# Kernel optimization log

Measured on AMD Instinct MI355X. Metric: run time of the kernel, lower is better.

## Reference

```python
import jax, jax.numpy as jnp
import numpy as np

B, DIM, N, K, NA = 1, 64, 1024, 16, 12
POS_HID = 64
ATTN_HID = 4 * DIM


def setup_inputs() -> dict:
    key = jax.random.key(0)
    ks = jax.random.split(key, 8)
    s = 0.05  # small init scale, mimics xavier magnitude
    return {
        "xyz": jax.random.normal(ks[0], (B, 3, N), jnp.float32),
        "feats": jax.random.normal(ks[1], (B, DIM, N, NA), jnp.float32),
        "anchors": jax.random.normal(ks[2], (NA, 3, 3), jnp.float32),
        "to_qkv": jax.random.normal(ks[3], (3 * DIM, DIM), jnp.float32) * s,
        "pos_mlp1": jax.random.normal(ks[4], (POS_HID, 3), jnp.float32) * s,
        "pos_mlp2": jax.random.normal(ks[5], (DIM, POS_HID), jnp.float32) * s,
        "attn_mlp1": jax.random.normal(ks[6], (ATTN_HID, DIM), jnp.float32) * s,
        "attn_mlp2": jax.random.normal(ks[7], (DIM, ATTN_HID), jnp.float32) * s,
    }


def reference(xyz, feats, anchors, to_qkv, pos_mlp1, pos_mlp2, attn_mlp1, attn_mlp2):
    # --- KNN over points (self included) ---
    pts = jnp.swapaxes(xyz, 1, 2)                      # [B,N,3]
    sq = jnp.sum(pts * pts, axis=-1)                   # [B,N]
    d2 = sq[:, :, None] + sq[:, None, :] - 2.0 * jnp.einsum('bnd,bmd->bnm', pts, pts)
    _, idx = jax.lax.top_k(-d2, K)                     # [B,N,K] nearest indices

    # --- gather helpers (vmapped over batch) ---
    gather3 = jax.vmap(lambda x, i: x[:, i])           # [C,N],[N,K] -> [C,N,K]
    gather4 = jax.vmap(lambda x, i: x[:, i, :])        # [C,N,A],[N,K] -> [C,N,K,A]

    # --- relative positions rotated by anchors ---
    grouped_xyz = gather3(xyz, idx)                    # [B,3,N,K]
    rel = xyz[:, :, :, None] - grouped_xyz             # [B,3,N,K]
    gx = jnp.einsum('aij,bjnk->binka', anchors, rel)   # [B,3,N,K,NA]

    # --- positional embedding MLP ---
    pe = jnp.einsum('ji,binka->bjnka', pos_mlp1, gx)   # [B,POS_HID,N,K,NA]
    pe = jax.nn.relu(pe)
    pe = jnp.einsum('ji,binka->bjnka', pos_mlp2, pe)   # [B,DIM,N,K,NA]

    # --- qkv projection ---
    qkv = jnp.einsum('ji,bina->bjna', to_qkv, feats)   # [B,3*DIM,N,NA]
    q, k, v = jnp.split(qkv, 3, axis=1)                # each [B,DIM,N,NA]

    k_g = gather4(k, idx)                              # [B,DIM,N,K,NA]
    v_g = gather4(v, idx) + pe                         # [B,DIM,N,K,NA]
    qk_rel = q[:, :, :, None, :] - k_g                 # [B,DIM,N,K,NA]

    # --- attention MLP on (qk_rel + pe) ---
    sim = qk_rel + pe
    sim = jnp.einsum('ji,binka->bjnka', attn_mlp1, sim)  # [B,4*DIM,N,K,NA]
    sim = jax.nn.relu(sim)
    sim = jnp.einsum('ji,binka->bjnka', attn_mlp2, sim)  # [B,DIM,N,K,NA]

    # --- per-channel softmax over neighbor axis, aggregate ---
    attn = jax.nn.softmax(sim, axis=-2)
    return jnp.sum(attn * v_g, axis=-2)                # [B,DIM,N,NA]
```

## Files before the change

### kernel.cpp

```cpp
#include <hip/hip_runtime.h>

#define NPTS 1024
#define DIM 64
#define KNN 16
#define NA 12
#define NCOL 192
#define XPAD 72

typedef __attribute__((ext_vector_type(8))) short bf16x8;
typedef __attribute__((ext_vector_type(4))) float f32x4;

static __device__ inline unsigned short f2bfu(float x) {
    __bf16 b = (__bf16)x;
    return __builtin_bit_cast(unsigned short, b);
}
static __device__ inline float bf2f(unsigned short s) {
    return __uint_as_float(((unsigned)s) << 16);
}
static __device__ inline unsigned pk2(float lo, float hi) {
    return (unsigned)f2bfu(lo) | ((unsigned)f2bfu(hi) << 16);
}
static __device__ inline bf16x8 load8_cvt(const float* p) {
    f32x4 u = *(const f32x4*)p;
    f32x4 v = *(const f32x4*)(p + 4);
    bf16x8 r;
    r[0] = (short)f2bfu(u[0]); r[1] = (short)f2bfu(u[1]); r[2] = (short)f2bfu(u[2]); r[3] = (short)f2bfu(u[3]);
    r[4] = (short)f2bfu(v[0]); r[5] = (short)f2bfu(v[1]); r[6] = (short)f2bfu(v[2]); r[7] = (short)f2bfu(v[3]);
    return r;
}

__global__ __launch_bounds__(256) void prep_kernel(const float* __restrict__ feats,
                                                   const float* __restrict__ to_qkv,
                                                   float* __restrict__ qkvT,
                                                   unsigned short* __restrict__ pack,
                                                   const float* __restrict__ pos2,
                                                   const float* __restrict__ am1,
                                                   const float* __restrict__ am2,
                                                   const float* __restrict__ xyz,
                                                   int* __restrict__ idxout) {
    __shared__ unsigned short XT[48][72];
    __shared__ float px[NPTS], py[NPTS], pz[NPTS];
    const int t = threadIdx.x;
    const int n0 = blockIdx.x * 48;

    if (blockIdx.x < 72 && t < 64) {
        int s = blockIdx.x;
        int c16p = t & 15, gp = t >> 4;
        const float* src;
        if (s < 8) {
            int nt = s >> 1, kt = s & 1;
            src = pos2 + (nt * 16 + c16p) * 64 + kt * 32 + gp * 8;
        } else if (s < 40) {
            int u = s - 8, hq = u >> 3, nt = (u >> 1) & 3, kt = u & 1;
            src = am1 + (hq * 64 + nt * 16 + c16p) * 64 + kt * 32 + gp * 8;
        } else {
            int u = s - 40, hq = u >> 3, nt = (u >> 1) & 3, kt = u & 1;
            src = am2 + (nt * 16 + c16p) * 256 + hq * 64 + kt * 32 + gp * 8;
        }
        unsigned short* dst = pack + (s * 64 + t) * 8;
        #pragma unroll
        for (int e = 0; e < 8; ++e) dst[e] = f2bfu(src[e]);
    }

    for (int m = t; m < NPTS; m += 256) {
        px[m] = xyz[m];
        py[m] = xyz[NPTS + m];
        pz[m] = xyz[2 * NPTS + m];
    }
    for (int e = t; e < 48 * 64; e += 256) {
        int c = e % 48, i = e / 48;
        XT[c][i] = f2bfu(feats[i * (NPTS * NA) + n0 + c]);
    }
    __syncthreads();

    const int lane = t & 63, w = t >> 6, c16 = lane & 15, g = lane >> 4;

    {
        bf16x8 bfr[3][2];
        #pragma unroll
        for (int ni = 0; ni < 3; ++ni)
            #pragma unroll
            for (int kt = 0; kt < 2; ++kt) {
                int cd = (w * 3 + ni) * 16 + c16;
                bfr[ni][kt] = load8_cvt(to_qkv + cd * 64 + kt * 32 + g * 8);
            }
        const f32x4 zero4 = {0.f, 0.f, 0.f, 0.f};
        #pragma unroll
        for (int mt = 0; mt < 3; ++mt) {
            f32x4 acc[3] = {zero4, zero4, zero4};
            #pragma unroll
            for (int kt = 0; kt < 2; ++kt) {
                bf16x8 af = *(const bf16x8*)&XT[mt * 16 + c16][kt * 32 + g * 8];
                #pragma unroll
                for (int ni = 0; ni < 3; ++ni)
                    acc[ni] = __builtin_amdgcn_mfma_f32_16x16x32_bf16(af, bfr[ni][kt], acc[ni], 0, 0, 0);
            }
            #pragma unroll
            for (int ni = 0; ni < 3; ++ni) {
                int cd = (w * 3 + ni) * 16 + c16;
                int c = cd >> 6, d = cd & 63;
                #pragma unroll
                for (int r = 0; r < 4; ++r) {
                    int na = n0 + mt * 16 + 4 * g + r;
                    qkvT[c * (NPTS * NA * DIM) + na * 64 + d] = acc[ni][r];
                }
            }
        }
    }

    {
        const int n = blockIdx.x * 4 + w;
        const float xn = px[n], yn = py[n], zn = pz[n];
        const float sqn = xn * xn + yn * yn + zn * zn;
        float dd[16]; int id[16];
        #pragma unroll
        for (int j = 0; j < 16; ++j) {
            int m = j * 64 + lane;
            float xm = px[m], ym = py[m], zm = pz[m];
            float sqm = xm * xm + ym * ym + zm * zm;
            float dot = xn * xm + yn * ym + zn * zm;
            dd[j] = sqn + sqm - 2.f * dot;
            id[j] = m;
        }
        for (int r = 0; r < KNN; ++r) {
            float bd = 1e30f; int bi = 0x7fffffff;
            #pragma unroll
            for (int j = 0; j < 16; ++j)
                if (dd[j] < bd || (dd[j] == bd && id[j] < bi)) { bd = dd[j]; bi = id[j]; }
            #pragma unroll
            for (int mask = 1; mask < 64; mask <<= 1) {
                float od = __shfl_xor(bd, mask);
                int oi = __shfl_xor(bi, mask);
                if (od < bd || (od == bd && oi < bi)) { bd = od; bi = oi; }
            }
            if (lane == 0) idxout[n * KNN + r] = bi;
            #pragma unroll
            for (int j = 0; j < 16; ++j)
                if (id[j] == bi) dd[j] = 1e30f;
        }
    }
}

__global__ __launch_bounds__(384, 3) void attn_main(const float* __restrict__ xyz,
                                                    const float* __restrict__ pos1,
                                                    const float* __restrict__ anchors,
                                                    const unsigned short* __restrict__ pack,
                                                    const float* __restrict__ qT,
                                                    const float* __restrict__ kT,
                                                    const float* __restrict__ vT,
                                                    const int* __restrict__ nn,
                                                    float* __restrict__ out) {
    __shared__ float P1s[192];
    __shared__ float abs_s[108];
    __shared__ __align__(16) unsigned short Xw[6 * 32 * XPAD];

    const int n = blockIdx.x, t = threadIdx.x;
    const int lane = t & 63, wave = t >> 6;
    const int c16 = lane & 15, g = lane >> 4;
    const int a0 = 2 * wave;

    if (t < 192) P1s[t] = pos1[t];
    if (t < 108) abs_s[t] = anchors[t];
    __syncthreads();

    int mk[4];
    #pragma unroll
    for (int r = 0; r < 4; ++r) mk[r] = nn[n * KNN + 4 * g + r];
    const int mc = nn[n * KNN + c16];
    const float relx = xyz[n] - xyz[mc];
    const float rely = xyz[NPTS + n] - xyz[NPTS + mc];
    const float relz = xyz[2 * NPTS + n] - xyz[2 * NPTS + mc];

    float G[2][3];
    #pragma unroll
    for (int ai = 0; ai < 2; ++ai) {
        int a = a0 + ai;
        G[ai][0] = abs_s[a * 9 + 0] * relx + abs_s[a * 9 + 1] * rely + abs_s[a * 9 + 2] * relz;
        G[ai][1] = abs_s[a * 9 + 3] * relx + abs_s[a * 9 + 4] * rely + abs_s[a * 9 + 5] * relz;
        G[ai][2] = abs_s[a * 9 + 6] * relx + abs_s[a * 9 + 7] * rely + abs_s[a * 9 + 8] * relz;
    }
    bf16x8 pfrag[2][2];
    #pragma unroll
    for (int kt = 0; kt < 2; ++kt)
        #pragma unroll
        for (int e = 0; e < 8; ++e) {
            int h = kt * 32 + g * 8 + e;
            float p0 = P1s[3 * h], p1 = P1s[3 * h + 1], p2 = P1s[3 * h + 2];
            #pragma unroll
            for (int ai = 0; ai < 2; ++ai) {
                float p = p0 * G[ai][0] + p1 * G[ai][1] + p2 * G[ai][2];
                pfrag[ai][kt][e] = (short)f2bfu(fmaxf(p, 0.f));
            }
        }

    const bf16x8* pk16 = (const bf16x8*)pack;
    const f32x4 zero4 = {0.f, 0.f, 0.f, 0.f};

    f32x4 acc[2][4];
    #pragma unroll
    for (int ai = 0; ai < 2; ++ai)
        #pragma unroll
        for (int nt = 0; nt < 4; ++nt) acc[ai][nt] = zero4;
    #pragma unroll
    for (int kt = 0; kt < 2; ++kt)
        #pragma unroll
        for (int nt = 0; nt < 4; ++nt) {
            bf16x8 bf = pk16[(nt * 2 + kt) * 64 + lane];
            acc[0][nt] = __builtin_amdgcn_mfma_f32_16x16x32_bf16(pfrag[0][kt], bf, acc[0][nt], 0, 0, 0);
            acc[1][nt] = __builtin_amdgcn_mfma_f32_16x16x32_bf16(pfrag[1][kt], bf, acc[1][nt], 0, 0, 0);
        }

    unsigned short* xw = Xw + wave * 32 * XPAD;
    unsigned vgp[2][4][2];
    #pragma unroll
    for (int ai = 0; ai < 2; ++ai) {
        int a = a0 + ai;
        #pragma unroll
        for (int nt = 0; nt < 4; ++nt) {
            int d = nt * 16 + c16;
            float qv = qT[(n * NA + a) * DIM + d];
            float xr[4], vg[4];
            #pragma unroll
            for (int r = 0; r < 4; ++r) {
                int b = (mk[r] * NA + a) * DIM + d;
                float pe = acc[ai][nt][r];
                xr[r] = qv - kT[b] + pe;
                vg[r] = vT[b] + pe;
            }
            vgp[ai][nt][0] = pk2(vg[0], vg[1]);
            vgp[ai][nt][1] = pk2(vg[2], vg[3]);
            #pragma unroll
            for (int r = 0; r < 4; ++r)
                xw[(ai * 16 + 4 * g + r) * XPAD + d] = f2bfu(xr[r]);
        }
    }
    __builtin_amdgcn_sched_barrier(0);
    asm volatile("s_waitcnt lgkmcnt(0)" ::: "memory");
    __builtin_amdgcn_sched_barrier(0);

    bf16x8 xf[2][2];
    #pragma unroll
    for (int ai = 0; ai < 2; ++ai)
        #pragma unroll
        for (int kt = 0; kt < 2; ++kt)
            xf[ai][kt] = *(const bf16x8*)&xw[(ai * 16 + c16) * XPAD + kt * 32 + g * 8];

    f32x4 sacc[2][4];
    #pragma unroll
    for (int ai = 0; ai < 2; ++ai)
        #pragma unroll
        for (int nt = 0; nt < 4; ++nt) sacc[ai][nt] = zero4;

    for (int hq = 0; hq < 4; ++hq) {
        f32x4 hacc[2][4];
        #pragma unroll
        for (int ai = 0; ai < 2; ++ai)
            #pragma unroll
            for (int nt = 0; nt < 4; ++nt) hacc[ai][nt] = zero4;
        #pragma unroll
        for (int kt = 0; kt < 2; ++kt)
            #pragma unroll
            for (int nt = 0; nt < 4; ++nt) {
                bf16x8 bf = pk16[(8 + hq * 8 + nt * 2 + kt) * 64 + lane];
                hacc[0][nt] = __builtin_amdgcn_mfma_f32_16x16x32_bf16(xf[0][kt], bf, hacc[0][nt], 0, 0, 0);
                hacc[1][nt] = __builtin_amdgcn_mfma_f32_16x16x32_bf16(xf[1][kt], bf, hacc[1][nt], 0, 0, 0);
            }
        #pragma unroll
        for (int ai = 0; ai < 2; ++ai)
            #pragma unroll
            for (int nt = 0; nt < 4; ++nt) {
                int col = nt * 16 + c16;
                #pragma unroll
                for (int r = 0; r < 4; ++r)
                    xw[(ai * 16 + 4 * g + r) * XPAD + col] = f2bfu(fmaxf(hacc[ai][nt][r], 0.f));
            }
        __builtin_amdgcn_sched_barrier(0);
        asm volatile("s_waitcnt lgkmcnt(0)" ::: "memory");
        __builtin_amdgcn_sched_barrier(0);
        bf16x8 hf[2][2];
        #pragma unroll
        for (int ai = 0; ai < 2; ++ai)
            #pragma unroll
            for (int kt = 0; kt < 2; ++kt)
                hf[ai][kt] = *(const bf16x8*)&xw[(ai * 16 + c16) * XPAD + kt * 32 + g * 8];
        #pragma unroll
        for (int kt = 0; kt < 2; ++kt)
            #pragma unroll
            for (int nt = 0; nt < 4; ++nt) {
                bf16x8 bf = pk16[(40 + hq * 8 + nt * 2 + kt) * 64 + lane];
                sacc[0][nt] = __builtin_amdgcn_mfma_f32_16x16x32_bf16(hf[0][kt], bf, sacc[0][nt], 0, 0, 0);
                sacc[1][nt] = __builtin_amdgcn_mfma_f32_16x16x32_bf16(hf[1][kt], bf, sacc[1][nt], 0, 0, 0);
            }
    }

    #pragma unroll
    for (int ai = 0; ai < 2; ++ai) {
        int a = a0 + ai;
        #pragma unroll
        for (int nt = 0; nt < 4; ++nt) {
            int d = nt * 16 + c16;
            float e0 = __expf(sacc[ai][nt][0]);
            float e1 = __expf(sacc[ai][nt][1]);
            float e2 = __expf(sacc[ai][nt][2]);
            float e3 = __expf(sacc[ai][nt][3]);
            float den = (e0 + e1) + (e2 + e3);
            unsigned v01 = vgp[ai][nt][0], v23 = vgp[ai][nt][1];
            float num = (e0 * bf2f((unsigned short)(v01 & 0xffff)) + e1 * bf2f((unsigned short)(v01 >> 16)))
                      + (e2 * bf2f((unsigned short)(v23 & 0xffff)) + e3 * bf2f((unsigned short)(v23 >> 16)));
            den += __shfl_xor(den, 16); num += __shfl_xor(num, 16);
            den += __shfl_xor(den, 32); num += __shfl_xor(num, 32);
            if (g == 0)
                out[(d * NPTS + n) * NA + a] = num / den;
        }
    }
}

extern "C" void kernel_launch(void* const* d_in, const int* in_sizes, int n_in,
                              void* d_out, int out_size, void* d_ws, size_t ws_size,
                              hipStream_t stream) {
    const float* xyz     = (const float*)d_in[0];
    const float* feats   = (const float*)d_in[1];
    const float* anchors = (const float*)d_in[2];
    const float* to_qkv  = (const float*)d_in[3];
    const float* pos1    = (const float*)d_in[4];
    const float* pos2    = (const float*)d_in[5];
    const float* am1     = (const float*)d_in[6];
    const float* am2     = (const float*)d_in[7];
    float* out = (float*)d_out;

    float* ws = (float*)d_ws;
    const int seg = NPTS * NA * DIM;
    float* qT = ws;
    float* kT = ws + seg;
    float* vT = ws + 2 * seg;
    int* nn = (int*)(ws + 3 * seg);
    unsigned short* pack = (unsigned short*)(ws + 3 * seg + NPTS * KNN);

    prep_kernel<<<256, 256, 0, stream>>>(feats, to_qkv, qT, pack, pos2, am1, am2, xyz, nn);
    attn_main<<<NPTS, 384, 0, stream>>>(xyz, pos1, anchors, pack, qT, kT, vT, nn, out);
}
```

Before: 90.32 us.

## Split prep kernel into more blocks and drop explicit LDS waitcnt barriers

The prep kernel now launches 768 blocks that each project 16 point-anchor rows instead of 256 blocks doing 48 rows. KNN runs only in the first 256 blocks, and the other blocks skip loading xyz into shared memory. The aim is more parallelism and less per-block serial work in the QKV projection. Separately, the explicit s_waitcnt lgkmcnt(0) and sched barriers between LDS writes and reads in attn_main are removed, leaving ordering to the compiler, which could be unsafe if it relied on them for cross-lane LDS visibility.

```diff
diff --git a/kernel.cpp b/kernel.cpp
--- a/kernel.cpp
+++ b/kernel.cpp
@@ -4,7 +4,6 @@
 #define DIM 64
 #define KNN 16
 #define NA 12
-#define NCOL 192
 #define XPAD 72
 
 typedef __attribute__((ext_vector_type(8))) short bf16x8;
@@ -38,13 +37,15 @@
                                                    const float* __restrict__ am2,
                                                    const float* __restrict__ xyz,
                                                    int* __restrict__ idxout) {
-    __shared__ unsigned short XT[48][72];
+    __shared__ unsigned short XT[16][72];
     __shared__ float px[NPTS], py[NPTS], pz[NPTS];
+    const int b = blockIdx.x;
     const int t = threadIdx.x;
-    const int n0 = blockIdx.x * 48;
-
-    if (blockIdx.x < 72 && t < 64) {
-        int s = blockIdx.x;
+    const int n0 = b * 16;
+    const bool do_knn = (b < 256);
+
+    if (b < 72 && t < 64) {
+        int s = b;
         int c16p = t & 15, gp = t >> 4;
         const float* src;
         if (s < 8) {
@@ -62,13 +63,15 @@
         for (int e = 0; e < 8; ++e) dst[e] = f2bfu(src[e]);
     }
 
-    for (int m = t; m < NPTS; m += 256) {
-        px[m] = xyz[m];
-        py[m] = xyz[NPTS + m];
-        pz[m] = xyz[2 * NPTS + m];
-    }
-    for (int e = t; e < 48 * 64; e += 256) {
-        int c = e % 48, i = e / 48;
+    if (do_knn) {
+        for (int m = t; m < NPTS; m += 256) {
+            px[m] = xyz[m];
+            py[m] = xyz[NPTS + m];
+            pz[m] = xyz[2 * NPTS + m];
+        }
+    }
+    for (int e = t; e < 16 * 64; e += 256) {
+        int c = e & 15, i = e >> 4;
         XT[c][i] = f2bfu(feats[i * (NPTS * NA) + n0 + c]);
     }
     __syncthreads();
@@ -76,40 +79,32 @@
     const int lane = t & 63, w = t >> 6, c16 = lane & 15, g = lane >> 4;
 
     {
-        bf16x8 bfr[3][2];
-        #pragma unroll
-        for (int ni = 0; ni < 3; ++ni)
-            #pragma unroll
-            for (int kt = 0; kt < 2; ++kt) {
-                int cd = (w * 3 + ni) * 16 + c16;
-                bfr[ni][kt] = load8_cvt(to_qkv + cd * 64 + kt * 32 + g * 8);
-            }
         const f32x4 zero4 = {0.f, 0.f, 0.f, 0.f};
-        #pragma unroll
-        for (int mt = 0; mt < 3; ++mt) {
-            f32x4 acc[3] = {zero4, zero4, zero4};
-            #pragma unroll
-            for (int kt = 0; kt < 2; ++kt) {
-                bf16x8 af = *(const bf16x8*)&XT[mt * 16 + c16][kt * 32 + g * 8];
-                #pragma unroll
-                for (int ni = 0; ni < 3; ++ni)
-                    acc[ni] = __builtin_amdgcn_mfma_f32_16x16x32_bf16(af, bfr[ni][kt], acc[ni], 0, 0, 0);
-            }
+        f32x4 acc[3] = {zero4, zero4, zero4};
+        #pragma unroll
+        for (int kt = 0; kt < 2; ++kt) {
+            bf16x8 af = *(const bf16x8*)&XT[c16][kt * 32 + g * 8];
             #pragma unroll
             for (int ni = 0; ni < 3; ++ni) {
                 int cd = (w * 3 + ni) * 16 + c16;
-                int c = cd >> 6, d = cd & 63;
-                #pragma unroll
-                for (int r = 0; r < 4; ++r) {
-                    int na = n0 + mt * 16 + 4 * g + r;
-                    qkvT[c * (NPTS * NA * DIM) + na * 64 + d] = acc[ni][r];
-                }
-            }
-        }
-    }
-
-    {
-        const int n = blockIdx.x * 4 + w;
+                bf16x8 bfr = load8_cvt(to_qkv + cd * 64 + kt * 32 + g * 8);
+                acc[ni] = __builtin_amdgcn_mfma_f32_16x16x32_bf16(af, bfr, acc[ni], 0, 0, 0);
+            }
+        }
+        #pragma unroll
+        for (int ni = 0; ni < 3; ++ni) {
+            int cd = (w * 3 + ni) * 16 + c16;
+            int c = cd >> 6, d = cd & 63;
+            #pragma unroll
+            for (int r = 0; r < 4; ++r) {
+                int na = n0 + 4 * g + r;
+                qkvT[c * (NPTS * NA * DIM) + na * 64 + d] = acc[ni][r];
+            }
+        }
+    }
+
+    if (do_knn) {
+        const int n = b * 4 + w;
         const float xn = px[n], yn = py[n], zn = pz[n];
         const float sqn = xn * xn + yn * yn + zn * zn;
         float dd[16]; int id[16];
@@ -234,9 +229,6 @@
                 xw[(ai * 16 + 4 * g + r) * XPAD + d] = f2bfu(xr[r]);
         }
     }
-    __builtin_amdgcn_sched_barrier(0);
-    asm volatile("s_waitcnt lgkmcnt(0)" ::: "memory");
-    __builtin_amdgcn_sched_barrier(0);
 
     bf16x8 xf[2][2];
     #pragma unroll
@@ -274,9 +266,6 @@
                 for (int r = 0; r < 4; ++r)
                     xw[(ai * 16 + 4 * g + r) * XPAD + col] = f2bfu(fmaxf(hacc[ai][nt][r], 0.f));
             }
-        __builtin_amdgcn_sched_barrier(0);
-        asm volatile("s_waitcnt lgkmcnt(0)" ::: "memory");
-        __builtin_amdgcn_sched_barrier(0);
         bf16x8 hf[2][2];
         #pragma unroll
         for (int ai = 0; ai < 2; ++ai)
@@ -336,6 +325,6 @@
     int* nn = (int*)(ws + 3 * seg);
     unsigned short* pack = (unsigned short*)(ws + 3 * seg + NPTS * KNN);
 
-    prep_kernel<<<256, 256, 0, stream>>>(feats, to_qkv, qT, pack, pos2, am1, am2, xyz, nn);
+    prep_kernel<<<768, 256, 0, stream>>>(feats, to_qkv, qT, pack, pos2, am1, am2, xyz, nn);
     attn_main<<<NPTS, 384, 0, stream>>>(xyz, pos1, anchors, pack, qT, kT, vT, nn, out);
 }
```

Result: slower. 108.4 us (+20.0%).
